# Kernel optimization log

Measured on AMD Instinct MI355X. Metric: run time of the kernel, lower is better.

The kernel has to match this reference:

```python
import jax, jax.numpy as jnp
import numpy as np

COUT, CIN = 1024, 1024  # self.shape = (cout, cin) in the torch module
NNZ = 131072


def setup_inputs() -> dict:
    key = jax.random.key(0)
    k_x, k_v, k_r, k_c = jax.random.split(key, 4)
    x = jax.random.normal(k_x, (4, 4096, CIN), dtype=jnp.float32)
    values = jax.random.normal(k_v, (NNZ,), dtype=jnp.float32)
    rows = jax.random.randint(k_r, (NNZ,), 0, COUT, dtype=jnp.int32)
    cols = jax.random.randint(k_c, (NNZ,), 0, CIN, dtype=jnp.int32)
    indices = jnp.stack([rows, cols], axis=0)  # [2, nnz], integer-valued
    return {"x": x, "values": values, "indices": indices}


def reference(x, values, indices):
    # torch: sparse_coo_tensor(indices, values, (cout, cin)).coalesce();
    # coalescing sums duplicate (row, col) entries -> scatter-add densify.
    rows, cols = indices[0], indices[1]
    W = jnp.zeros((COUT, CIN), dtype=values.dtype).at[rows, cols].add(values)
    # 3D path: out[b, l, co] = sum_ci W[co, ci] * x[b, l, ci]
    return jnp.einsum('blc,oc->blo', x, W)
```

## Files before the change

kernel.cpp:

```cpp
#include <hip/hip_runtime.h>
#include <cstdint>
#include <cstddef>

#define CIN  1024
#define COUT 1024

typedef __attribute__((ext_vector_type(8))) short bf16x8;
typedef __attribute__((ext_vector_type(4))) float f32x4;

__device__ __forceinline__ unsigned short f2bf(float f) {
    union { float f; unsigned int i; } v;
    v.f = f;
    unsigned int u = v.i;
    u += 0x7FFFu + ((u >> 16) & 1u);
    return (unsigned short)(u >> 16);
}

__global__ void zero_f32(float4* __restrict__ p) {
    p[blockIdx.x * 256 + threadIdx.x] = float4{0.f, 0.f, 0.f, 0.f};
}

__global__ void scatter_add(const float* __restrict__ vals,
                            const int* __restrict__ rows,
                            const int* __restrict__ cols,
                            float* __restrict__ W, int nnz) {
    int i = blockIdx.x * 256 + threadIdx.x;
    if (i < nnz) {
        atomicAdd(W + (size_t)rows[i] * CIN + cols[i], vals[i]);
    }
}

__global__ void cvt_bf16_bulk(const float* __restrict__ src, unsigned short* __restrict__ dst) {
    size_t i = ((size_t)blockIdx.x * 256 + threadIdx.x) * 8;
    float4 v0 = *(const float4*)(src + i);
    float4 v1 = *(const float4*)(src + i + 4);
    union { bf16x8 v; unsigned short u[8]; } w;
    w.u[0] = f2bf(v0.x); w.u[1] = f2bf(v0.y); w.u[2] = f2bf(v0.z); w.u[3] = f2bf(v0.w);
    w.u[4] = f2bf(v1.x); w.u[5] = f2bf(v1.y); w.u[6] = f2bf(v1.z); w.u[7] = f2bf(v1.w);
    *(bf16x8*)(dst + i) = w.v;
}


#define GLD16(SRC_, DST_)                                                     \
  __builtin_amdgcn_global_load_lds(                                           \
      (const __attribute__((address_space(1))) void*)(SRC_),                  \
      (__attribute__((address_space(3))) void*)(DST_), 16, 0, 0)

#define STAGE_A(BUF_, HALF_, KT_) do {                                        \
    GLD16(pa + (size_t)((HALF_) * 128)      * CIN + (size_t)(KT_) * 64,       \
          As + (BUF_) * 16384 + ((HALF_) * 128) * 64 + tid8);                 \
    GLD16(pa + (size_t)((HALF_) * 128 + 64) * CIN + (size_t)(KT_) * 64,       \
          As + (BUF_) * 16384 + ((HALF_) * 128 + 64) * 64 + tid8);            \
  } while (0)

#define STAGE_B(BUF_, HALF_, KT_) do {                                        \
    GLD16(pb + (size_t)((HALF_) * 128)      * CIN + (size_t)(KT_) * 64,       \
          Bs + (BUF_) * 16384 + ((HALF_) * 128) * 64 + tid8);                 \
    GLD16(pb + (size_t)((HALF_) * 128 + 64) * CIN + (size_t)(KT_) * 64,       \
          Bs + (BUF_) * 16384 + ((HALF_) * 128 + 64) * 64 + tid8);            \
  } while (0)

#define PHASE(BUF_, QA_, QB_, STAGE_BODY_, CKPT_BODY_) do {                   \
    bf16x8 af[2][4];                                                          \
    bf16x8 bfr[2][2];                                                         \
    const unsigned short* abase_ =                                            \
        As + (BUF_) * 16384 + ((QA_) * 128 + wm64) * 64;                      \
    const unsigned short* bbase_ =                                            \
        Bs + (BUF_) * 16384 + ((QB_) * 128 + wn32) * 64;                      \
    _Pragma("unroll")                                                         \
    for (int ks_ = 0; ks_ < 2; ++ks_) {                                       \
      const int cx_ = ((ks_ * 4 + quad) ^ s7) * 8;                            \
      _Pragma("unroll")                                                       \
      for (int mf_ = 0; mf_ < 4; ++mf_)                                       \
        af[ks_][mf_] = *(const bf16x8*)(abase_ + (mf_ * 16 + l16) * 64 + cx_);\
      _Pragma("unroll")                                                       \
      for (int nf_ = 0; nf_ < 2; ++nf_)                                       \
        bfr[ks_][nf_] = *(const bf16x8*)(bbase_ + (nf_ * 16 + l16) * 64 + cx_);\
    }                                                                         \
    STAGE_BODY_                                                               \
    __builtin_amdgcn_s_barrier();                                             \
    asm volatile("s_waitcnt lgkmcnt(0)" ::: "memory");                        \
    __builtin_amdgcn_sched_barrier(0);                                        \
    __builtin_amdgcn_s_setprio(1);                                            \
    _Pragma("unroll")                                                         \
    for (int ks_ = 0; ks_ < 2; ++ks_)                                         \
      _Pragma("unroll")                                                       \
      for (int mf_ = 0; mf_ < 4; ++mf_)                                       \
        _Pragma("unroll")                                                     \
        for (int nf_ = 0; nf_ < 2; ++nf_)                                     \
          acc[QA_][QB_][mf_][nf_] = __builtin_amdgcn_mfma_f32_16x16x32_bf16(  \
              af[ks_][mf_], bfr[ks_][nf_], acc[QA_][QB_][mf_][nf_], 0, 0, 0); \
    __builtin_amdgcn_s_setprio(0);                                            \
    CKPT_BODY_                                                                \
    __builtin_amdgcn_s_barrier();                                             \
  } while (0)

__global__ __launch_bounds__(512, 2) void gemm_8ph(
    const unsigned short* __restrict__ A,
    const unsigned short* __restrict__ B,
    float* __restrict__ C,
    int M) {
    (void)M;
    constexpr int K = CIN;

    __shared__ __align__(16) unsigned short As[2 * 16384];
    __shared__ __align__(16) unsigned short Bs[2 * 16384];

    const int tid  = threadIdx.x;
    const int lane = tid & 63;
    const int w    = tid >> 6;
    const int quad = lane >> 4;
    const int l16  = lane & 15;
    const int s7   = l16 & 7;
    const int wm64 = (w >> 2) * 64;
    const int wn32 = (w & 3) * 32;

    const int rowA0 = blockIdx.x * 256;
    const int rowB0 = blockIdx.y * 256;

    const int stg_row = tid >> 3;
    const int c_data  = (tid & 7) ^ (stg_row & 7);
    const int tid8    = tid * 8;
    const unsigned short* pa = A + (size_t)(rowA0 + stg_row) * K + c_data * 8;
    const unsigned short* pb = B + (size_t)(rowB0 + stg_row) * K + c_data * 8;

    f32x4 acc[2][2][4][2] = {};

    STAGE_A(0, 0, 0); STAGE_A(0, 1, 0); STAGE_B(0, 0, 0); STAGE_B(0, 1, 0);
    STAGE_A(1, 0, 1); STAGE_B(1, 0, 1);
    asm volatile("s_waitcnt vmcnt(4)" ::: "memory");
    __builtin_amdgcn_s_barrier();

#pragma unroll 1
    for (int i = 0; i < 8; ++i) {
        const int  k1 = 2 * i + 1;
        const int  k2 = 2 * i + 2;
        const int  k3 = 2 * i + 3;
        const bool nl = (i < 7);

        PHASE(0, 0, 0, STAGE_A(1, 1, k1); STAGE_B(1, 1, k1); , );
        PHASE(0, 0, 1, , );
        PHASE(0, 1, 0, if (nl) STAGE_A(0, 0, k2); , );
        PHASE(0, 1, 1, if (nl) STAGE_B(0, 0, k2); ,
              if (nl) { asm volatile("s_waitcnt vmcnt(4)" ::: "memory"); }
              else    { asm volatile("s_waitcnt vmcnt(0)" ::: "memory"); } );
        PHASE(1, 0, 0, if (nl) { STAGE_A(0, 1, k2); STAGE_B(0, 1, k2); } , );
        PHASE(1, 0, 1, , );
        PHASE(1, 1, 0, if (nl) STAGE_A(1, 0, k3); , );
        PHASE(1, 1, 1, if (nl) STAGE_B(1, 0, k3); ,
              if (nl) { asm volatile("s_waitcnt vmcnt(4)" ::: "memory"); } );
    }

#pragma unroll
    for (int qa = 0; qa < 2; ++qa)
#pragma unroll
        for (int qb = 0; qb < 2; ++qb)
#pragma unroll
            for (int mf = 0; mf < 4; ++mf)
#pragma unroll
                for (int nf = 0; nf < 2; ++nf) {
                    const int row0 = rowA0 + qa * 128 + wm64 + mf * 16 + quad * 4;
                    float* cp = C + (size_t)row0 * COUT
                                  + rowB0 + qb * 128 + wn32 + nf * 16 + l16;
#pragma unroll
                    for (int r = 0; r < 4; ++r)
                        cp[(size_t)r * COUT] = acc[qa][qb][mf][nf][r];
                }
}

extern "C" void kernel_launch(void* const* d_in, const int* in_sizes, int n_in,
                              void* d_out, int out_size, void* d_ws, size_t ws_size,
                              hipStream_t stream) {
    const float* x    = (const float*)d_in[0];
    const float* vals = (const float*)d_in[1];
    const int*   idx  = (const int*)d_in[2];

    float* out = (float*)d_out;

    const int nnz = in_sizes[2] / 2;
    const int M   = in_sizes[0] / CIN;

    const size_t wf_bytes = (size_t)COUT * CIN * sizeof(float);
    const size_t wb_bytes = (size_t)COUT * CIN * sizeof(unsigned short);

    float*          Wf = (float*)d_ws;
    unsigned short* Wb = (unsigned short*)((char*)d_ws + wf_bytes);
    unsigned short* Xb = (unsigned short*)((char*)d_ws + wf_bytes + wb_bytes);

    zero_f32<<<dim3(COUT * CIN / (256 * 4)), dim3(256), 0, stream>>>((float4*)Wf);
    scatter_add<<<dim3((nnz + 255) / 256), dim3(256), 0, stream>>>(vals, idx, idx + nnz, Wf, nnz);
    cvt_bf16_bulk<<<dim3(COUT * CIN / (256 * 8)), dim3(256), 0, stream>>>(Wf, Wb);
    cvt_bf16_bulk<<<dim3((unsigned)((size_t)M * CIN / (256 * 8))), dim3(256), 0, stream>>>(x, Xb);
    gemm_8ph<<<dim3(M / 256, COUT / 256), dim3(512), 0, stream>>>(Xb, Wb, out, M);
}
```

Baseline: 165.1 us.

## Reuse LDS fragments across phases and reorder global-to-LDS staging

Each 8-phase K-step now keeps A and B register fragments alive across quadrant phases, using two B fragment sets (bf0/bf1). A and B are reloaded from LDS only when the quadrant changes, instead of being reloaded for every phase. This cuts LDS read traffic per MFMA. The order in which half-tiles are staged into LDS is also changed so B halves are issued earlier, and the ordering constraints differ. The extra live fragments raise register pressure, and correctness now depends on the new stage and wait ordering lining up with the buffer reuse.

```diff
diff --git a/kernel.cpp b/kernel.cpp
--- a/kernel.cpp
+++ b/kernel.cpp
@@ -60,28 +60,29 @@
           Bs + (BUF_) * 16384 + ((HALF_) * 128 + 64) * 64 + tid8);            \
   } while (0)
 
-#define PHASE(BUF_, QA_, QB_, STAGE_BODY_, CKPT_BODY_) do {                   \
-    bf16x8 af[2][4];                                                          \
-    bf16x8 bfr[2][2];                                                         \
-    const unsigned short* abase_ =                                            \
-        As + (BUF_) * 16384 + ((QA_) * 128 + wm64) * 64;                      \
-    const unsigned short* bbase_ =                                            \
-        Bs + (BUF_) * 16384 + ((QB_) * 128 + wn32) * 64;                      \
+#define LOAD_A(BUF_, QA_) do {                                                \
+    const unsigned short* ab_ = As + (BUF_) * 16384 + ((QA_) * 128 + wm64) * 64; \
     _Pragma("unroll")                                                         \
     for (int ks_ = 0; ks_ < 2; ++ks_) {                                       \
       const int cx_ = ((ks_ * 4 + quad) ^ s7) * 8;                            \
       _Pragma("unroll")                                                       \
       for (int mf_ = 0; mf_ < 4; ++mf_)                                       \
-        af[ks_][mf_] = *(const bf16x8*)(abase_ + (mf_ * 16 + l16) * 64 + cx_);\
+        af[ks_][mf_] = *(const bf16x8*)(ab_ + (mf_ * 16 + l16) * 64 + cx_);   \
+    }                                                                         \
+  } while (0)
+
+#define LOAD_B(BUF_, QB_, DST_) do {                                          \
+    const unsigned short* bb_ = Bs + (BUF_) * 16384 + ((QB_) * 128 + wn32) * 64; \
+    _Pragma("unroll")                                                         \
+    for (int ks_ = 0; ks_ < 2; ++ks_) {                                       \
+      const int cx_ = ((ks_ * 4 + quad) ^ s7) * 8;                            \
       _Pragma("unroll")                                                       \
       for (int nf_ = 0; nf_ < 2; ++nf_)                                       \
-        bfr[ks_][nf_] = *(const bf16x8*)(bbase_ + (nf_ * 16 + l16) * 64 + cx_);\
+        DST_[ks_][nf_] = *(const bf16x8*)(bb_ + (nf_ * 16 + l16) * 64 + cx_); \
     }                                                                         \
-    STAGE_BODY_                                                               \
-    __builtin_amdgcn_s_barrier();                                             \
-    asm volatile("s_waitcnt lgkmcnt(0)" ::: "memory");                        \
-    __builtin_amdgcn_sched_barrier(0);                                        \
-    __builtin_amdgcn_s_setprio(1);                                            \
+  } while (0)
+
+#define MFMA_Q(QA_, QB_, BF_)                                                 \
     _Pragma("unroll")                                                         \
     for (int ks_ = 0; ks_ < 2; ++ks_)                                         \
       _Pragma("unroll")                                                       \
@@ -89,11 +90,16 @@
         _Pragma("unroll")                                                     \
         for (int nf_ = 0; nf_ < 2; ++nf_)                                     \
           acc[QA_][QB_][mf_][nf_] = __builtin_amdgcn_mfma_f32_16x16x32_bf16(  \
-              af[ks_][mf_], bfr[ks_][nf_], acc[QA_][QB_][mf_][nf_], 0, 0, 0); \
-    __builtin_amdgcn_s_setprio(0);                                            \
-    CKPT_BODY_                                                                \
+              af[ks_][mf_], BF_[ks_][nf_], acc[QA_][QB_][mf_][nf_], 0, 0, 0)
+
+#define SYNC_PRE() do {                                                       \
     __builtin_amdgcn_s_barrier();                                             \
-  } while (0)
+    asm volatile("s_waitcnt lgkmcnt(0)" ::: "memory");                        \
+    __builtin_amdgcn_sched_barrier(0);                                        \
+    __builtin_amdgcn_s_setprio(1);                                            \
+  } while (0)
+
+#define SYNC_POST() __builtin_amdgcn_s_setprio(0)
 
 __global__ __launch_bounds__(512, 2) void gemm_8ph(
     const unsigned short* __restrict__ A,
@@ -126,7 +132,7 @@
 
     f32x4 acc[2][2][4][2] = {};
 
-    STAGE_A(0, 0, 0); STAGE_A(0, 1, 0); STAGE_B(0, 0, 0); STAGE_B(0, 1, 0);
+    STAGE_A(0, 0, 0); STAGE_B(0, 0, 0); STAGE_B(0, 1, 0); STAGE_A(0, 1, 0);
     STAGE_A(1, 0, 1); STAGE_B(1, 0, 1);
     asm volatile("s_waitcnt vmcnt(4)" ::: "memory");
     __builtin_amdgcn_s_barrier();
@@ -138,17 +144,43 @@
         const int  k3 = 2 * i + 3;
         const bool nl = (i < 7);
 
-        PHASE(0, 0, 0, STAGE_A(1, 1, k1); STAGE_B(1, 1, k1); , );
-        PHASE(0, 0, 1, , );
-        PHASE(0, 1, 0, if (nl) STAGE_A(0, 0, k2); , );
-        PHASE(0, 1, 1, if (nl) STAGE_B(0, 0, k2); ,
-              if (nl) { asm volatile("s_waitcnt vmcnt(4)" ::: "memory"); }
-              else    { asm volatile("s_waitcnt vmcnt(0)" ::: "memory"); } );
-        PHASE(1, 0, 0, if (nl) { STAGE_A(0, 1, k2); STAGE_B(0, 1, k2); } , );
-        PHASE(1, 0, 1, , );
-        PHASE(1, 1, 0, if (nl) STAGE_A(1, 0, k3); , );
-        PHASE(1, 1, 1, if (nl) STAGE_B(1, 0, k3); ,
-              if (nl) { asm volatile("s_waitcnt vmcnt(4)" ::: "memory"); } );
+        bf16x8 af[2][4];
+        bf16x8 bf0[2][2], bf1[2][2];
+
+        LOAD_A(0, 0); LOAD_B(0, 0, bf0);
+        STAGE_B(1, 1, k1);
+        SYNC_PRE(); MFMA_Q(0, 0, bf0); SYNC_POST();
+        __builtin_amdgcn_s_barrier();
+        LOAD_B(0, 1, bf1);
+        STAGE_A(1, 1, k1);
+        SYNC_PRE(); MFMA_Q(0, 1, bf1); SYNC_POST();
+        __builtin_amdgcn_s_barrier();
+        LOAD_A(0, 1);
+        if (nl) STAGE_A(0, 0, k2);
+        SYNC_PRE(); MFMA_Q(1, 0, bf0); SYNC_POST();
+        __builtin_amdgcn_s_barrier();
+        if (nl) STAGE_B(0, 0, k2);
+        SYNC_PRE(); MFMA_Q(1, 1, bf1); SYNC_POST();
+        if (nl) { asm volatile("s_waitcnt vmcnt(4)" ::: "memory"); }
+        else    { asm volatile("s_waitcnt vmcnt(0)" ::: "memory"); }
+        __builtin_amdgcn_s_barrier();
+
+        LOAD_A(1, 0); LOAD_B(1, 0, bf0);
+        if (nl) STAGE_B(0, 1, k2);
+        SYNC_PRE(); MFMA_Q(0, 0, bf0); SYNC_POST();
+        __builtin_amdgcn_s_barrier();
+        LOAD_B(1, 1, bf1);
+        if (nl) STAGE_A(0, 1, k2);
+        SYNC_PRE(); MFMA_Q(0, 1, bf1); SYNC_POST();
+        __builtin_amdgcn_s_barrier();
+        LOAD_A(1, 1);
+        if (nl) STAGE_A(1, 0, k3);
+        SYNC_PRE(); MFMA_Q(1, 0, bf0); SYNC_POST();
+        __builtin_amdgcn_s_barrier();
+        if (nl) STAGE_B(1, 0, k3);
+        SYNC_PRE(); MFMA_Q(1, 1, bf1); SYNC_POST();
+        if (nl) { asm volatile("s_waitcnt vmcnt(4)" ::: "memory"); }
+        __builtin_amdgcn_s_barrier();
     }
 
 #pragma unroll
```

Measured after the change: 161.3 us. 2.4% less time.
